# Performance work log

Measured on AMD Instinct MI355X. Metric: run time of the kernel, lower is better.

Reference implementation:

```python
import jax, jax.numpy as jnp
import numpy as np

N, E, D_IN, D, L = 50000, 800000, 128, 256, 3
BN_EPS = 1e-5


def _bn(x, gamma, beta):
    # torch BatchNorm1d training-mode forward: biased batch statistics over node dim
    m = x.mean(axis=0)
    v = x.var(axis=0)  # ddof=0, matches torch normalization
    return gamma * (x - m) * jax.lax.rsqrt(v + BN_EPS) + beta


def setup_inputs() -> dict:
    key = jax.random.key(0)
    ks = jax.random.split(key, 12)
    s_in = 1.0 / np.sqrt(D_IN)
    s_d = 1.0 / np.sqrt(D)
    s_2d = 1.0 / np.sqrt(2 * D)
    return {
        "pre_node_emb": jax.random.normal(ks[0], (1, N, D_IN), jnp.float32),
        "edge_index": jax.random.randint(ks[1], (1, E, 2), 0, N, jnp.int64),
        "W0": jax.random.uniform(ks[2], (D_IN, D), jnp.float32, -s_in, s_in),
        "b0": jax.random.uniform(ks[3], (D,), jnp.float32, -s_in, s_in),
        "W1": jax.random.uniform(ks[4], (L, D, 2 * D), jnp.float32, -s_d, s_d),
        "b1": jax.random.uniform(ks[5], (L, 2 * D), jnp.float32, -s_d, s_d),
        "g1": jnp.ones((L, 2 * D), jnp.float32),
        "beta1": jnp.zeros((L, 2 * D), jnp.float32),
        "W2": jax.random.uniform(ks[6], (L, 2 * D, D), jnp.float32, -s_2d, s_2d),
        "b2": jax.random.uniform(ks[7], (L, D), jnp.float32, -s_2d, s_2d),
        "gf": jnp.ones((L, D), jnp.float32),
        "betaf": jnp.zeros((L, D), jnp.float32),
    }


def reference(pre_node_emb, edge_index, W0, b0, W1, b1, g1, beta1, W2, b2, gf, betaf):
    x = pre_node_emb[0]            # [N, D_IN]
    ei = edge_index[0]             # [E, 2] -> transposed in torch; rows are (src, dst)
    src, dst = ei[:, 0], ei[:, 1]
    x = x @ W0 + b0                # node embedder -> [N, D]
    for l in range(L):
        # GINConv (eps=0): sum-aggregate neighbor messages, then MLP
        agg = jax.ops.segment_sum(x[src], dst, num_segments=N)   # scatter-add
        h = x + agg
        h = h @ W1[l] + b1[l]
        h = _bn(h, g1[l], beta1[l])
        h = jax.nn.relu(h)
        h = h @ W2[l] + b2[l]
        x = _bn(h + x, gf[l], betaf[l])  # residual + outer BatchNorm
    return x
```

## Files before the change

### kernel.cpp

```cpp
#include <hip/hip_runtime.h>

#define MNODES 50000
#define M_PAD  50048
#define NEDGES 800000
#define DIN    128
#define DD     256
#define D2     512
#define NLAYERS 3
#define BN_EPS 1e-5f
#define NREP   16

typedef unsigned short ushort_t;
typedef __bf16 v8bf __attribute__((ext_vector_type(8)));
typedef unsigned short v8us __attribute__((ext_vector_type(8)));
typedef float  v4f  __attribute__((ext_vector_type(4)));

#define GLOBAL_AS __attribute__((address_space(1)))
#define LDS_AS    __attribute__((address_space(3)))

__device__ __forceinline__ float bf2f(ushort_t u) {
    unsigned x = ((unsigned)u) << 16;
    return __uint_as_float(x);
}
__device__ __forceinline__ ushort_t f2bf(float f) {
    unsigned u = __float_as_uint(f);
    u += 0x7FFF + ((u >> 16) & 1);
    return (ushort_t)(u >> 16);
}
__device__ __forceinline__ void async16(const ushort_t* g, ushort_t* l) {
    __builtin_amdgcn_global_load_lds((const GLOBAL_AS unsigned int*)g,
                                     (LDS_AS unsigned int*)l, 16, 0, 0);
}
#define BARRIER() asm volatile("s_barrier" ::: "memory")

#define R0 (M_PAD * DIN)
#define RW (DIN * DD + 2 * NLAYERS * DD * D2)
#define NSTATZ (NREP * D2 * 2 + NREP * DD * 2)
__global__ void k_prep_all(const float* __restrict__ pre, ushort_t* __restrict__ preb,
                           const float* __restrict__ W0, const float* __restrict__ W1,
                           const float* __restrict__ W2,
                           ushort_t* __restrict__ W0T, ushort_t* __restrict__ W1T,
                           ushort_t* __restrict__ W2T,
                           float* __restrict__ caf, float* __restrict__ ccf,
                           float* __restrict__ statz, int* __restrict__ deg) {
    int i = blockIdx.x * blockDim.x + threadIdx.x;
    if (i < R0) {
        int row = i >> 7;
        preb[i] = f2bf(row < MNODES ? pre[i] : 0.f);
        return;
    }
    int j = i - R0;
    if (j < RW) {
        if (j < DIN * DD) {
            int n = j >> 7, k = j & 127;
            W0T[j] = f2bf(W0[k * DD + n]);
        } else if (j < DIN * DD + NLAYERS * DD * D2) {
            int j2 = j - DIN * DD;
            int l = j2 >> 17, off = j2 & 131071;
            int n = off >> 8, k = off & 255;
            W1T[(size_t)l * 131072 + off] = f2bf(W1[(size_t)l * 131072 + k * D2 + n]);
        } else {
            int j2 = j - DIN * DD - NLAYERS * DD * D2;
            int l = j2 >> 17, off = j2 & 131071;
            int n = off >> 9, k = off & 511;
            W2T[(size_t)l * 131072 + off] = f2bf(W2[(size_t)l * 131072 + k * DD + n]);
        }
        return;
    }
    j -= RW;
    if (j < 256) { caf[j] = 1.f; ccf[j] = 0.f; return; }
    j -= 256;
    if (j < NSTATZ) { statz[j] = 0.f; return; }
    j -= NSTATZ;
    if (j < MNODES) deg[j] = 0;
}

__global__ void k_hist(const int* __restrict__ ei, int* __restrict__ deg) {
    int e = blockIdx.x * blockDim.x + threadIdx.x;
    if (e < NEDGES) atomicAdd(&deg[ei[e * 2 + 1]], 1);
}
__global__ void k_scan1(const int* __restrict__ deg, int* __restrict__ rowptr,
                        int* __restrict__ bsum, int n) {
    __shared__ int tmp[256];
    int tid = threadIdx.x;
    int i = blockIdx.x * 256 + tid;
    int v = (i < n) ? deg[i] : 0;
    tmp[tid] = v;
    __syncthreads();
    #pragma unroll
    for (int off = 1; off < 256; off <<= 1) {
        int t = (tid >= off) ? tmp[tid - off] : 0;
        __syncthreads();
        tmp[tid] += t;
        __syncthreads();
    }
    if (i < n) rowptr[i + 1] = tmp[tid];
    if (tid == 255) bsum[blockIdx.x] = tmp[255];
}
__global__ __launch_bounds__(256)
void k_scan2(int* __restrict__ bsum, int nb) {
    __shared__ int tmp[256];
    int tid = threadIdx.x;
    int v = (tid < nb) ? bsum[tid] : 0;
    tmp[tid] = v;
    __syncthreads();
    #pragma unroll
    for (int off = 1; off < 256; off <<= 1) {
        int t = (tid >= off) ? tmp[tid - off] : 0;
        __syncthreads();
        tmp[tid] += t;
        __syncthreads();
    }
    if (tid < nb) bsum[tid] = tmp[tid] - v;
}
__global__ void k_scan3(const int* __restrict__ deg, const int* __restrict__ bsum,
                        int* __restrict__ rowptr, int* __restrict__ cursor, int n) {
    int i = blockIdx.x * 256 + threadIdx.x;
    if (i == 0) rowptr[0] = 0;
    if (i < n) {
        int incl = rowptr[i + 1] + bsum[i >> 8];
        rowptr[i + 1] = incl;
        cursor[i] = incl - deg[i];
    }
}
__global__ void k_fill(const int* __restrict__ ei, int* __restrict__ cursor,
                       int* __restrict__ col) {
    int e = blockIdx.x * blockDim.x + threadIdx.x;
    if (e < NEDGES) {
        int pos = atomicAdd(&cursor[ei[e * 2 + 1]], 1);
        col[pos] = ei[e * 2];
    }
}

__global__ void k_gather(const int* __restrict__ rowptr, const int* __restrict__ col,
                         const ushort_t* __restrict__ x, const float* __restrict__ ca,
                         const float* __restrict__ cc, ushort_t* __restrict__ out) {
    int node = blockIdx.x * 4 + (threadIdx.x >> 6);
    int lane = threadIdx.x & 63;
    if (node >= MNODES) return;
    const ushort4* xp = (const ushort4*)x;
    ushort4 v = xp[(size_t)node * 64 + lane];
    float a0 = bf2f(v.x), a1 = bf2f(v.y), a2 = bf2f(v.z), a3 = bf2f(v.w);
    int s = rowptr[node], e = rowptr[node + 1];
    int i = s;
    for (; i + 7 < e; i += 8) {
        ushort4 u[8];
        #pragma unroll
        for (int j = 0; j < 8; j++) u[j] = xp[(size_t)col[i + j] * 64 + lane];
        #pragma unroll
        for (int j = 0; j < 8; j++) {
            a0 += bf2f(u[j].x); a1 += bf2f(u[j].y);
            a2 += bf2f(u[j].z); a3 += bf2f(u[j].w);
        }
    }
    for (; i < e; i++) {
        ushort4 u = xp[(size_t)col[i] * 64 + lane];
        a0 += bf2f(u.x); a1 += bf2f(u.y); a2 += bf2f(u.z); a3 += bf2f(u.w);
    }
    int c = lane * 4;
    float dn = (float)(e - s) + 1.0f;
    ushort4 o;
    o.x = f2bf(ca[c + 0] * a0 + dn * cc[c + 0]);
    o.y = f2bf(ca[c + 1] * a1 + dn * cc[c + 1]);
    o.z = f2bf(ca[c + 2] * a2 + dn * cc[c + 2]);
    o.w = f2bf(ca[c + 3] * a3 + dn * cc[c + 3]);
    ((ushort4*)out)[(size_t)node * 64 + lane] = o;
}

__global__ void k_coeffs(float* __restrict__ sums, float* __restrict__ sumsq,
                         const float* __restrict__ g, const float* __restrict__ beta,
                         float* __restrict__ ca, float* __restrict__ cc,
                         float2* __restrict__ cacc, int n) {
    int c = blockIdx.x * blockDim.x + threadIdx.x;
    if (c >= n) return;
    float s = 0.f, q = 0.f;
    #pragma unroll
    for (int r = 0; r < NREP; r++) {
        s += sums[r * n + c];  sums[r * n + c]  = 0.f;
        q += sumsq[r * n + c]; sumsq[r * n + c] = 0.f;
    }
    float mean = s * (1.0f / MNODES);
    float var  = q * (1.0f / MNODES) - mean * mean;
    float a    = g[c] * rsqrtf(var + BN_EPS);
    float b    = beta[c] - a * mean;
    ca[c] = a;
    cc[c] = b;
    if (cacc) cacc[c] = make_float2(a, b);
}

__global__ void k_apply_out(const ushort_t* __restrict__ h, const float* __restrict__ ca,
                            const float* __restrict__ cc, float* __restrict__ out) {
    int i = blockIdx.x * blockDim.x + threadIdx.x;
    if (i >= MNODES * 64) return;
    int c = (i & 63) * 4;
    ushort4 v = ((const ushort4*)h)[i];
    float4 o;
    o.x = ca[c + 0] * bf2f(v.x) + cc[c + 0];
    o.y = ca[c + 1] * bf2f(v.y) + cc[c + 1];
    o.z = ca[c + 2] * bf2f(v.z) + cc[c + 2];
    o.w = ca[c + 3] * bf2f(v.w) + cc[c + 3];
    ((float4*)out)[i] = o;
}

template<int DO_STATS, int RES, int FUSE_BN, int KT>
__global__ __launch_bounds__(256, 3)
void k_gemm_bf(const ushort_t* __restrict__ A, const ushort_t* __restrict__ WT,
               const float* __restrict__ bias,
               const ushort_t* resid, const float* __restrict__ r_ca,
               const float* __restrict__ r_cc, const float2* __restrict__ cacc,
               ushort_t* out, float* __restrict__ sums, float* __restrict__ sumsq,
               int M, int N) {
    static_assert(KT % 128 == 0, "KT multiple of 128");
    __shared__ __align__(16) ushort_t Bs[128 * 128];
    const int tid = threadIdx.x;
    const int w = tid >> 6, lane = tid & 63;
    const int quad = lane >> 4, l15 = lane & 15;

    const int nxb = N >> 7;
    const int nwg = nxb * (int)gridDim.y;
    const int orig = (int)blockIdx.y * nxb + (int)blockIdx.x;
    const int qq = nwg >> 3, rr = nwg & 7, xc = orig & 7, oi = orig >> 3;
    const int swz = (xc < rr ? xc * (qq + 1) : rr * (qq + 1) + (xc - rr) * qq) + oi;
    const int bx = swz & (nxb - 1);
    const int by = (nxb == 4) ? (swz >> 2) : (swz >> 1);
    const int m0 = by * 128, n0 = bx * 128;

    float2* cacc_lds = nullptr;
    if constexpr (FUSE_BN != 0) {
        __shared__ __align__(16) float2 cacc_s[KT];
        cacc_lds = cacc_s;
        #pragma unroll
        for (int k2 = tid; k2 < KT; k2 += 256) cacc_lds[k2] = cacc[k2];
    }

    const ushort_t* srcB[8];
    {
        int r4 = lane >> 4, s15 = lane & 15;
        #pragma unroll
        for (int j = 0; j < 8; j++) {
            int gi = j * 4 + w;
            int rowb = gi * 4 + r4;
            int gc = s15 ^ (rowb & 15);
            srcB[j] = WT + (size_t)(n0 + rowb) * KT + gc * 8;
        }
    }

    const ushort_t* Ap = A + (size_t)(m0 + w * 32 + l15) * KT + quad * 8;

    v4f acc[2][8];
    #pragma unroll
    for (int i = 0; i < 2; i++)
        #pragma unroll
        for (int j = 0; j < 8; j++)
            acc[i][j] = (v4f){0.f, 0.f, 0.f, 0.f};

    constexpr int nk = KT >> 5;
    constexpr int nc = KT >> 7;

    v8bf aE[2], aO[2];
    #pragma unroll
    for (int mt = 0; mt < 2; mt++) aE[mt] = *(const v8bf*)(Ap + mt * 16 * KT);
    #pragma unroll
    for (int mt = 0; mt < 2; mt++) aO[mt] = *(const v8bf*)(Ap + mt * 16 * KT + 32);

    #pragma unroll
    for (int j = 0; j < 8; j++)
        async16(srcB[j], &Bs[(j * 4 + w) * 512]);
    __syncthreads();

    #pragma unroll
    for (int c = 0; c < nc; c++) {
        if (c > 0) {
            BARRIER();
            #pragma unroll
            for (int j = 0; j < 8; j++)
                async16(srcB[j] + c * 128, &Bs[(j * 4 + w) * 512]);
            __syncthreads();
        }
        #pragma unroll
        for (int tl = 0; tl < 4; tl++) {
            const int s = c * 4 + tl;
            v8bf bb[8];
            #pragma unroll
            for (int nt = 0; nt < 8; nt++) {
                int n_l = nt * 16 + l15;
                int slot = (tl * 4 + quad) ^ (n_l & 15);
                bb[nt] = *(const v8bf*)&Bs[n_l * 128 + slot * 8];
            }
            v8bf aUse[2];
            if (s & 1) { aUse[0] = aO[0]; aUse[1] = aO[1]; }
            else       { aUse[0] = aE[0]; aUse[1] = aE[1]; }
            if (s + 2 < nk) {
                if (s & 1) {
                    #pragma unroll
                    for (int mt = 0; mt < 2; mt++)
                        aO[mt] = *(const v8bf*)(Ap + mt * 16 * KT + (s + 2) * 32);
                } else {
                    #pragma unroll
                    for (int mt = 0; mt < 2; mt++)
                        aE[mt] = *(const v8bf*)(Ap + mt * 16 * KT + (s + 2) * 32);
                }
            }
            if constexpr (FUSE_BN != 0) {
                const float* cb = (const float*)&cacc_lds[(s << 5) + (quad << 3)];
                #pragma unroll
                for (int mt = 0; mt < 2; mt++) {
                    v8us au = *(v8us*)&aUse[mt];
                    v8bf o;
                    #pragma unroll
                    for (int j = 0; j < 8; j++) {
                        float h = bf2f(au[j]);
                        o[j] = (__bf16)fmaxf(fmaf(cb[2 * j], h, cb[2 * j + 1]), 0.f);
                    }
                    aUse[mt] = o;
                }
            }
            #pragma unroll
            for (int mt = 0; mt < 2; mt++)
                #pragma unroll
                for (int nt = 0; nt < 8; nt++)
                    acc[mt][nt] = __builtin_amdgcn_mfma_f32_16x16x32_bf16(
                        aUse[mt], bb[nt], acc[mt][nt], 0, 0, 0);
        }
    }

    const int mlim = M - m0;
    float s_sum[8], s_sq[8];
    #pragma unroll
    for (int nt = 0; nt < 8; nt++) { s_sum[nt] = 0.f; s_sq[nt] = 0.f; }
    #pragma unroll
    for (int nt = 0; nt < 8; nt++) {
        int colg = n0 + nt * 16 + l15;
        float bia = bias[colg];
        float rca = 0.f, rcc = 0.f;
        if (RES) { rca = r_ca[colg]; rcc = r_cc[colg]; }
        #pragma unroll
        for (int mt = 0; mt < 2; mt++) {
            int rbase = w * 32 + mt * 16 + quad * 4;
            #pragma unroll
            for (int r = 0; r < 4; r++) {
                int rl = rbase + r;
                if (rl < mlim) {
                    size_t idx = (size_t)(m0 + rl) * N + colg;
                    float v = acc[mt][nt][r] + bia;
                    if (RES) v += rca * bf2f(resid[idx]) + rcc;
                    out[idx] = f2bf(v);
                    if (DO_STATS) { s_sum[nt] += v; s_sq[nt] += v * v; }
                }
            }
        }
    }
    if (DO_STATS) {
        const int rep = (by * 4 + w) & (NREP - 1);
        #pragma unroll
        for (int nt = 0; nt < 8; nt++) {
            float s = s_sum[nt], q = s_sq[nt];
            s += __shfl_xor(s, 16); q += __shfl_xor(q, 16);
            s += __shfl_xor(s, 32); q += __shfl_xor(q, 32);
            if (quad == 0) {
                int colg = n0 + nt * 16 + l15;
                atomicAdd(&sums[rep * N + colg], s);
                atomicAdd(&sumsq[rep * N + colg], q);
            }
        }
    }
}

extern "C" void kernel_launch(void* const* d_in, const int* in_sizes, int n_in,
                              void* d_out, int out_size, void* d_ws, size_t ws_size,
                              hipStream_t stream) {
    const float* pre   = (const float*)d_in[0];
    const int*   ei    = (const int*)d_in[1];
    const float* W0    = (const float*)d_in[2];
    const float* b0    = (const float*)d_in[3];
    const float* W1    = (const float*)d_in[4];
    const float* b1    = (const float*)d_in[5];
    const float* g1    = (const float*)d_in[6];
    const float* beta1 = (const float*)d_in[7];
    const float* W2    = (const float*)d_in[8];
    const float* b2    = (const float*)d_in[9];
    const float* gf    = (const float*)d_in[10];
    const float* betaf = (const float*)d_in[11];

    char* p = (char*)d_ws;
    ushort_t* preb = (ushort_t*)p; p += (size_t)M_PAD * DIN * 2;
    ushort_t* ACT1 = (ushort_t*)p; p += (size_t)M_PAD * DD * 2;
    ushort_t* ACT2 = (ushort_t*)p; p += (size_t)M_PAD * DD * 2;
    ushort_t* H1   = (ushort_t*)p; p += (size_t)M_PAD * D2 * 2;
    ushort_t* W0T  = (ushort_t*)p; p += (size_t)DIN * DD * 2;
    ushort_t* W1T  = (ushort_t*)p; p += (size_t)NLAYERS * DD * D2 * 2;
    ushort_t* W2T  = (ushort_t*)p; p += (size_t)NLAYERS * D2 * DD * 2;
    float* sums1  = (float*)p; p += (size_t)NREP * D2 * 4;
    float* sumsq1 = (float*)p; p += (size_t)NREP * D2 * 4;
    float* sumsF  = (float*)p; p += (size_t)NREP * DD * 4;
    float* sumsqF = (float*)p; p += (size_t)NREP * DD * 4;
    float* ca1    = (float*)p; p += D2 * 4;
    float* cc1    = (float*)p; p += D2 * 4;
    float* caf    = (float*)p; p += DD * 4;
    float* ccf    = (float*)p; p += DD * 4;
    float2* cacc1 = (float2*)p; p += D2 * 8;
    int* deg    = (int*)p; p += (size_t)MNODES * 4;
    int* rowptr = (int*)p; p += (size_t)(MNODES + 1) * 4;
    int* cursor = (int*)p; p += (size_t)MNODES * 4;
    int* colx   = (int*)p; p += (size_t)NEDGES * 4;
    int* bsum   = (int*)p; p += 256 * 4;

    dim3 blk(256);
    const int mb = (MNODES + 127) / 128;
    const int nsb = (MNODES + 255) / 256;

    const int prep_total = R0 + RW + 256 + NSTATZ + MNODES;
    k_prep_all<<<(prep_total + 255) / 256, blk, 0, stream>>>(
        pre, preb, W0, W1, W2, W0T, W1T, W2T, caf, ccf, sums1, deg);

    k_hist<<<(NEDGES + 255) / 256, blk, 0, stream>>>(ei, deg);
    k_scan1<<<nsb, blk, 0, stream>>>(deg, rowptr, bsum, MNODES);
    k_scan2<<<1, blk, 0, stream>>>(bsum, nsb);
    k_scan3<<<nsb, blk, 0, stream>>>(deg, bsum, rowptr, cursor, MNODES);
    k_fill<<<(NEDGES + 255) / 256, blk, 0, stream>>>(ei, cursor, colx);

    k_gemm_bf<0, 0, 0, DIN><<<dim3(DD / 128, mb), blk, 0, stream>>>(
        preb, W0T, b0, nullptr, nullptr, nullptr, nullptr,
        ACT2, nullptr, nullptr, MNODES, DD);

    for (int l = 0; l < NLAYERS; l++) {
        k_gather<<<(MNODES + 3) / 4, blk, 0, stream>>>(rowptr, colx, ACT2, caf, ccf, ACT1);

        k_gemm_bf<1, 0, 0, DD><<<dim3(D2 / 128, mb), blk, 0, stream>>>(
            ACT1, W1T + (size_t)l * DD * D2, b1 + (size_t)l * D2,
            nullptr, nullptr, nullptr, nullptr,
            H1, sums1, sumsq1, MNODES, D2);
        k_coeffs<<<2, blk, 0, stream>>>(sums1, sumsq1, g1 + (size_t)l * D2,
                                        beta1 + (size_t)l * D2, ca1, cc1, cacc1, D2);

        k_gemm_bf<1, 1, 1, D2><<<dim3(DD / 128, mb), blk, 0, stream>>>(
            H1, W2T + (size_t)l * D2 * DD, b2 + (size_t)l * DD,
            ACT2, caf, ccf, cacc1,
            ACT2, sumsF, sumsqF, MNODES, DD);
        k_coeffs<<<1, blk, 0, stream>>>(sumsF, sumsqF, gf + (size_t)l * DD,
                                        betaf + (size_t)l * DD, caf, ccf, nullptr, DD);
    }

    k_apply_out<<<(MNODES * 64 + 255) / 256, blk, 0, stream>>>(ACT2, caf, ccf, (float*)d_out);
}
```

Measured before the change: 773.5 us.

## Double-buffer GEMM B tiles in LDS with finer waits and deeper A prefetch

The GEMM kernel now splits the B tile into two 64-wide K halves held in a double-buffered LDS array. The next half is loaded asynchronously while the current one is consumed, with explicit vmcnt waits in place of a full __syncthreads around every load. A-operand register prefetch goes from two steps ahead to four, and B fragment reads are split into two groups of four to cut register pressure. The prep kernel also converts the input embedding to bf16 with float4 vector loads; the trade-off is more registers for prefetch and more fragile hand-placed waitcnt logic.

```diff
diff --git a/kernel.cpp b/kernel.cpp
--- a/kernel.cpp
+++ b/kernel.cpp
@@ -32,8 +32,13 @@
                                      (LDS_AS unsigned int*)l, 16, 0, 0);
 }
 #define BARRIER() asm volatile("s_barrier" ::: "memory")
+#define VMWAIT8() asm volatile("s_waitcnt vmcnt(8)" ::: "memory")
+#define VMWAIT4() asm volatile("s_waitcnt vmcnt(4)" ::: "memory")
+#define VMWAIT0() asm volatile("s_waitcnt vmcnt(0)" ::: "memory")
+#define LGKM0()   asm volatile("s_waitcnt lgkmcnt(0)" ::: "memory")
 
 #define R0 (M_PAD * DIN)
+#define R0V (R0 / 4)
 #define RW (DIN * DD + 2 * NLAYERS * DD * D2)
 #define NSTATZ (NREP * D2 * 2 + NREP * DD * 2)
 __global__ void k_prep_all(const float* __restrict__ pre, ushort_t* __restrict__ preb,
@@ -44,12 +49,19 @@
                            float* __restrict__ caf, float* __restrict__ ccf,
                            float* __restrict__ statz, int* __restrict__ deg) {
     int i = blockIdx.x * blockDim.x + threadIdx.x;
-    if (i < R0) {
-        int row = i >> 7;
-        preb[i] = f2bf(row < MNODES ? pre[i] : 0.f);
+    if (i < R0V) {
+        int row = i >> 5;
+        ushort4 o;
+        if (row < MNODES) {
+            float4 v = ((const float4*)pre)[i];
+            o.x = f2bf(v.x); o.y = f2bf(v.y); o.z = f2bf(v.z); o.w = f2bf(v.w);
+        } else {
+            o.x = 0; o.y = 0; o.z = 0; o.w = 0;
+        }
+        ((ushort4*)preb)[i] = o;
         return;
     }
-    int j = i - R0;
+    int j = i - R0V;
     if (j < RW) {
         if (j < DIN * DD) {
             int n = j >> 7, k = j & 127;
@@ -202,6 +214,10 @@
     ((float4*)out)[i] = o;
 }
 
+#define LOADA(buf, st)                                                        \
+    { buf[0] = *(const v8bf*)(Ap + (st) * 32);                                \
+      buf[1] = *(const v8bf*)(Ap + 16 * KT + (st) * 32); }
+
 template<int DO_STATS, int RES, int FUSE_BN, int KT>
 __global__ __launch_bounds__(256, 3)
 void k_gemm_bf(const ushort_t* __restrict__ A, const ushort_t* __restrict__ WT,
@@ -211,7 +227,9 @@
                ushort_t* out, float* __restrict__ sums, float* __restrict__ sumsq,
                int M, int N) {
     static_assert(KT % 128 == 0, "KT multiple of 128");
-    __shared__ __align__(16) ushort_t Bs[128 * 128];
+    constexpr int nk  = KT >> 5;
+    constexpr int nc2 = KT >> 6;
+    __shared__ __align__(16) ushort_t Bs[2][128 * 64];
     const int tid = threadIdx.x;
     const int w = tid >> 6, lane = tid & 63;
     const int quad = lane >> 4, l15 = lane & 15;
@@ -233,15 +251,14 @@
         for (int k2 = tid; k2 < KT; k2 += 256) cacc_lds[k2] = cacc[k2];
     }
 
-    const ushort_t* srcB[8];
+    const ushort_t* srcB[4];
     {
-        int r4 = lane >> 4, s15 = lane & 15;
-        #pragma unroll
-        for (int j = 0; j < 8; j++) {
-            int gi = j * 4 + w;
-            int rowb = gi * 4 + r4;
-            int gc = s15 ^ (rowb & 15);
-            srcB[j] = WT + (size_t)(n0 + rowb) * KT + gc * 8;
+        int r8 = lane >> 3, s8 = lane & 7;
+        #pragma unroll
+        for (int j = 0; j < 4; j++) {
+            int rowb = (w * 4 + j) * 8 + r8;
+            int g = s8 ^ (rowb & 7);
+            srcB[j] = WT + (size_t)(n0 + rowb) * KT + g * 8;
         }
     }
 
@@ -254,52 +271,46 @@
         for (int j = 0; j < 8; j++)
             acc[i][j] = (v4f){0.f, 0.f, 0.f, 0.f};
 
-    constexpr int nk = KT >> 5;
-    constexpr int nc = KT >> 7;
-
-    v8bf aE[2], aO[2];
-    #pragma unroll
-    for (int mt = 0; mt < 2; mt++) aE[mt] = *(const v8bf*)(Ap + mt * 16 * KT);
-    #pragma unroll
-    for (int mt = 0; mt < 2; mt++) aO[mt] = *(const v8bf*)(Ap + mt * 16 * KT + 32);
-
-    #pragma unroll
-    for (int j = 0; j < 8; j++)
-        async16(srcB[j], &Bs[(j * 4 + w) * 512]);
-    __syncthreads();
-
-    #pragma unroll
-    for (int c = 0; c < nc; c++) {
+    v8bf a0[2], a1[2], a2[2], a3[2];
+    LOADA(a0, 0) LOADA(a1, 1) LOADA(a2, 2) LOADA(a3, 3)
+
+    #pragma unroll
+    for (int j = 0; j < 4; j++) async16(srcB[j], &Bs[0][(w * 4 + j) * 512]);
+    #pragma unroll
+    for (int j = 0; j < 4; j++) async16(srcB[j] + 64, &Bs[1][(w * 4 + j) * 512]);
+    if constexpr (FUSE_BN != 0) { LGKM0(); }
+    VMWAIT4();
+    BARRIER();
+
+    #pragma unroll
+    for (int c = 0; c < nc2; c++) {
         if (c > 0) {
             BARRIER();
-            #pragma unroll
-            for (int j = 0; j < 8; j++)
-                async16(srcB[j] + c * 128, &Bs[(j * 4 + w) * 512]);
-            __syncthreads();
-        }
-        #pragma unroll
-        for (int tl = 0; tl < 4; tl++) {
-            const int s = c * 4 + tl;
-            v8bf bb[8];
-            #pragma unroll
-            for (int nt = 0; nt < 8; nt++) {
-                int n_l = nt * 16 + l15;
-                int slot = (tl * 4 + quad) ^ (n_l & 15);
-                bb[nt] = *(const v8bf*)&Bs[n_l * 128 + slot * 8];
-            }
+            if (c + 1 < nc2) {
+                #pragma unroll
+                for (int j = 0; j < 4; j++)
+                    async16(srcB[j] + (c + 1) * 64, &Bs[(c + 1) & 1][(w * 4 + j) * 512]);
+                VMWAIT8();
+            } else {
+                VMWAIT0();
+            }
+            BARRIER();
+        }
+        const ushort_t* Bb = Bs[c & 1];
+        #pragma unroll
+        for (int tc = 0; tc < 2; tc++) {
+            const int s = c * 2 + tc;
+            const int sl4 = s & 3;
             v8bf aUse[2];
-            if (s & 1) { aUse[0] = aO[0]; aUse[1] = aO[1]; }
-            else       { aUse[0] = aE[0]; aUse[1] = aE[1]; }
-            if (s + 2 < nk) {
-                if (s & 1) {
-                    #pragma unroll
-                    for (int mt = 0; mt < 2; mt++)
-                        aO[mt] = *(const v8bf*)(Ap + mt * 16 * KT + (s + 2) * 32);
-                } else {
-                    #pragma unroll
-                    for (int mt = 0; mt < 2; mt++)
-                        aE[mt] = *(const v8bf*)(Ap + mt * 16 * KT + (s + 2) * 32);
-                }
+            if (sl4 == 0)      { aUse[0] = a0[0]; aUse[1] = a0[1]; }
+            else if (sl4 == 1) { aUse[0] = a1[0]; aUse[1] = a1[1]; }
+            else if (sl4 == 2) { aUse[0] = a2[0]; aUse[1] = a2[1]; }
+            else               { aUse[0] = a3[0]; aUse[1] = a3[1]; }
+            if (s + 4 < nk) {
+                if (sl4 == 0)      { LOADA(a0, s + 4) }
+                else if (sl4 == 1) { LOADA(a1, s + 4) }
+                else if (sl4 == 2) { LOADA(a2, s + 4) }
+                else               { LOADA(a3, s + 4) }
             }
             if constexpr (FUSE_BN != 0) {
                 const float* cb = (const float*)&cacc_lds[(s << 5) + (quad << 3)];
@@ -315,12 +326,32 @@
                     aUse[mt] = o;
                 }
             }
+            v8bf bb0[4];
+            #pragma unroll
+            for (int nt = 0; nt < 4; nt++) {
+                int n_l = nt * 16 + l15;
+                int slot = (tc * 4 + quad) ^ (n_l & 7);
+                bb0[nt] = *(const v8bf*)&Bb[n_l * 64 + slot * 8];
+            }
             #pragma unroll
             for (int mt = 0; mt < 2; mt++)
                 #pragma unroll
-                for (int nt = 0; nt < 8; nt++)
+                for (int nt = 0; nt < 4; nt++)
                     acc[mt][nt] = __builtin_amdgcn_mfma_f32_16x16x32_bf16(
-                        aUse[mt], bb[nt], acc[mt][nt], 0, 0, 0);
+                        aUse[mt], bb0[nt], acc[mt][nt], 0, 0, 0);
+            v8bf bb1[4];
+            #pragma unroll
+            for (int nt = 0; nt < 4; nt++) {
+                int n_l = (nt + 4) * 16 + l15;
+                int slot = (tc * 4 + quad) ^ (n_l & 7);
+                bb1[nt] = *(const v8bf*)&Bb[n_l * 64 + slot * 8];
+            }
+            #pragma unroll
+            for (int mt = 0; mt < 2; mt++)
+                #pragma unroll
+                for (int nt = 0; nt < 4; nt++)
+                    acc[mt][nt + 4] = __builtin_amdgcn_mfma_f32_16x16x32_bf16(
+                        aUse[mt], bb1[nt], acc[mt][nt + 4], 0, 0, 0);
         }
     }
 
@@ -409,7 +440,7 @@
     const int mb = (MNODES + 127) / 128;
     const int nsb = (MNODES + 255) / 256;
 
-    const int prep_total = R0 + RW + 256 + NSTATZ + MNODES;
+    const int prep_total = R0V + RW + 256 + NSTATZ + MNODES;
     k_prep_all<<<(prep_total + 255) / 256, blk, 0, stream>>>(
         pre, preb, W0, W1, W2, W0T, W1T, W2T, caf, ccf, sums1, deg);
 
```

Result: faster. 750.1 us (-3.0%).
